# Optimization experiments

Hardware: AMD Instinct MI355X
Metric: run time of the kernel (lower is better)

The kernel has to match this reference:

```python
import jax, jax.numpy as jnp
import numpy as np

DICT = 32768
TOP_K = 128
LN_EPS = 1e-5


def setup_inputs() -> dict:
    key = jax.random.key(0)
    k_x, k_we, k_be, k_wd, k_bd = jax.random.split(key, 5)
    B, S, D = 4, 2048, 768
    x = jax.random.normal(k_x, (B, S, D), dtype=jnp.float32)
    # nn.Linear stores weight as [out, in]; init scaled roughly like orthogonal gains
    W_enc = jax.random.normal(k_we, (DICT, D), dtype=jnp.float32) / np.sqrt(D)
    b_enc = jax.random.normal(k_be, (DICT,), dtype=jnp.float32) * 0.01
    W_dec = jax.random.normal(k_wd, (D, DICT), dtype=jnp.float32) * (0.1 / np.sqrt(DICT))
    b_dec = jax.random.normal(k_bd, (D,), dtype=jnp.float32) * 0.01
    ln_gamma = jnp.ones((DICT,), dtype=jnp.float32)
    ln_beta = jnp.zeros((DICT,), dtype=jnp.float32)
    return {"x": x, "W_enc": W_enc, "b_enc": b_enc, "ln_gamma": ln_gamma,
            "ln_beta": ln_beta, "W_dec": W_dec, "b_dec": b_dec}


def _layernorm(z, gamma, beta):
    mu = jnp.mean(z, axis=-1, keepdims=True)
    var = jnp.mean(jnp.square(z - mu), axis=-1, keepdims=True)
    return (z - mu) * jax.lax.rsqrt(var + LN_EPS) * gamma + beta


def _top_k_activation(z, k):
    # keep top-k values per row, zero elsewhere (scatter, like torch.scatter_)
    vals, idx = jax.lax.top_k(z, k)            # [B,S,k]
    out = jnp.zeros_like(z)
    return jnp.put_along_axis(out, idx, vals, axis=-1, inplace=False)


def reference(x, W_enc, b_enc, ln_gamma, ln_beta, W_dec, b_dec):
    # encoder: [B,S,D] @ [D,DICT] -> [B,S,DICT]
    z = jnp.einsum("bsd,fd->bsf", x, W_enc) + b_enc
    z = _layernorm(z, ln_gamma, ln_beta)
    z = jax.nn.relu(z)
    features = _top_k_activation(z, TOP_K)      # [B,S,DICT], mostly zero
    output = jnp.einsum("bsf,df->bsd", features, W_dec) + b_dec  # [B,S,D]
    return (output, features)
```

## Files before the change

kernel.cpp:

```cpp
#include <hip/hip_runtime.h>
#include <hip/hip_bf16.h>

#define R_TOT  8192
#define DIM    768
#define FDICT  32768
#define TOPK   128
#define LN_EPS 1e-5f
#define BAND_M 0.12f
#define BAND_CAP 192

using f32x4  = __attribute__((ext_vector_type(4))) float;
using short8 = __attribute__((ext_vector_type(8))) short;

__device__ inline short f2bf(float f) {
    __hip_bfloat16 h = __float2bfloat16(f);
    return *reinterpret_cast<short*>(&h);
}
__device__ inline float bf2f(short s) {
    return __uint_as_float(((unsigned)(unsigned short)s) << 16);
}
__device__ inline void load_lds16(const void* g, void* l) {
    __builtin_amdgcn_global_load_lds(
        (const __attribute__((address_space(1))) unsigned int*)g,
        (__attribute__((address_space(3))) unsigned int*)l, 16, 0, 0);
}

__global__ __launch_bounds__(256) void prep_fused(
    const float* __restrict__ x, const float* __restrict__ Wenc,
    const float* __restrict__ Wdec, const float* __restrict__ gamma,
    const float* __restrict__ beta, unsigned short* __restrict__ Xb,
    unsigned short* __restrict__ Wb, unsigned short* __restrict__ WdTb,
    float* __restrict__ gbinfo)
{
    __shared__ float tile[32][33];
    const int b = blockIdx.x;
    const int t = threadIdx.x;

    if (b < 1536) {
        const int n8 = R_TOT * DIM / 8;
        for (int g = b * 256 + t; g < n8; g += 1536 * 256) {
            const float4 a = ((const float4*)x)[g * 2];
            const float4 c = ((const float4*)x)[g * 2 + 1];
            short8 v;
            v[0] = f2bf(a.x); v[1] = f2bf(a.y); v[2] = f2bf(a.z); v[3] = f2bf(a.w);
            v[4] = f2bf(c.x); v[5] = f2bf(c.y); v[6] = f2bf(c.z); v[7] = f2bf(c.w);
            ((short8*)Xb)[g] = v;
        }
    } else if (b < 3584) {
        const int n8 = FDICT * DIM / 8;
        for (int g = (b - 1536) * 256 + t; g < n8; g += 2048 * 256) {
            const float4 a = ((const float4*)Wenc)[g * 2];
            const float4 c = ((const float4*)Wenc)[g * 2 + 1];
            short8 v;
            v[0] = f2bf(a.x); v[1] = f2bf(a.y); v[2] = f2bf(a.z); v[3] = f2bf(a.w);
            v[4] = f2bf(c.x); v[5] = f2bf(c.y); v[6] = f2bf(c.z); v[7] = f2bf(c.w);
            ((short8*)Wb)[g] = v;
        }
    } else if (b < 3584 + 24576) {
        const int b2 = b - 3584;
        const int fx = (b2 & 1023) * 32;
        const int dy = (b2 >> 10) * 32;
        const int tx = t & 31;
        const int ty = t >> 5;
        for (int i = ty; i < 32; i += 8)
            tile[i][tx] = Wdec[(size_t)(dy + i) * FDICT + fx + tx];
        __syncthreads();
        for (int i = ty; i < 32; i += 8)
            WdTb[(size_t)(fx + i) * DIM + dy + tx] = (unsigned short)f2bf(tile[tx][i]);
    } else {
        float* rr = &tile[0][0];
        const int w = t >> 6;
        float gmn = 1e30f, gmx = -1e30f, bmn = 1e30f, bmx = -1e30f;
        for (int i = t; i < FDICT / 4; i += 256) {
            const float4 g4 = ((const float4*)gamma)[i];
            const float4 b4 = ((const float4*)beta)[i];
            gmn = fminf(gmn, fminf(fminf(g4.x, g4.y), fminf(g4.z, g4.w)));
            gmx = fmaxf(gmx, fmaxf(fmaxf(g4.x, g4.y), fmaxf(g4.z, g4.w)));
            bmn = fminf(bmn, fminf(fminf(b4.x, b4.y), fminf(b4.z, b4.w)));
            bmx = fmaxf(bmx, fmaxf(fmaxf(b4.x, b4.y), fmaxf(b4.z, b4.w)));
        }
#pragma unroll
        for (int o = 32; o > 0; o >>= 1) {
            gmn = fminf(gmn, __shfl_down(gmn, o, 64));
            gmx = fmaxf(gmx, __shfl_down(gmx, o, 64));
            bmn = fminf(bmn, __shfl_down(bmn, o, 64));
            bmx = fmaxf(bmx, __shfl_down(bmx, o, 64));
        }
        if ((t & 63) == 0) {
            rr[w * 4 + 0] = gmn; rr[w * 4 + 1] = gmx;
            rr[w * 4 + 2] = bmn; rr[w * 4 + 3] = bmx;
        }
        __syncthreads();
        if (t == 0) {
            float a = rr[0], b_ = rr[1], c = rr[2], d = rr[3];
            for (int i = 1; i < 4; ++i) {
                a = fminf(a, rr[i * 4 + 0]); b_ = fmaxf(b_, rr[i * 4 + 1]);
                c = fminf(c, rr[i * 4 + 2]); d = fmaxf(d, rr[i * 4 + 3]);
            }
            gbinfo[0] = fmaxf(fabsf(a), fabsf(b_));
            gbinfo[1] = fmaxf(fabsf(c), fabsf(d));
            gbinfo[2] = (a == b_ && c == d) ? 1.f : 0.f;
            gbinfo[3] = b_;
            gbinfo[4] = d;
        }
    }
}

#define READ_A(P)                                                              \
    af00 = *(const short8*)&Sb[abase + (2*(P))*1024 + sw0];                    \
    af01 = *(const short8*)&Sb[abase + (2*(P))*1024 + sw1];                    \
    af10 = *(const short8*)&Sb[abase + (2*(P)+1)*1024 + sw0];                  \
    af11 = *(const short8*)&Sb[abase + (2*(P)+1)*1024 + sw1];

#define DO_MFMA(P)                                                             \
    __builtin_amdgcn_s_setprio(1);                                             \
    _Pragma("unroll")                                                          \
    for (int n = 0; n < 4; ++n) {                                              \
        acc[2*(P)][n]   = __builtin_amdgcn_mfma_f32_16x16x32_bf16(af00, bf0[n], acc[2*(P)][n],   0,0,0); \
        acc[2*(P)][n]   = __builtin_amdgcn_mfma_f32_16x16x32_bf16(af01, bf1[n], acc[2*(P)][n],   0,0,0); \
        acc[2*(P)+1][n] = __builtin_amdgcn_mfma_f32_16x16x32_bf16(af10, bf0[n], acc[2*(P)+1][n], 0,0,0); \
        acc[2*(P)+1][n] = __builtin_amdgcn_mfma_f32_16x16x32_bf16(af11, bf1[n], acc[2*(P)+1][n], 0,0,0); \
    }                                                                          \
    __builtin_amdgcn_s_setprio(0);

__global__ __launch_bounds__(512, 2) void enc_gemm(
    const unsigned short* __restrict__ Xb, const unsigned short* __restrict__ Wb,
    const float* __restrict__ benc, unsigned short* __restrict__ Zb,
    float* __restrict__ featZero)
{
    __shared__ __align__(16) unsigned short S[65536];

    const int t = threadIdx.x;
    const int w = t >> 6, l = t & 63;

    const int cpx = (int)gridDim.x >> 3;
    const int swz = ((int)blockIdx.x & 7) * cpx + ((int)blockIdx.x >> 3);
    const long bm = (long)(swz >> 7) * 256;
    const long bn = (long)(swz & 127) * 256;

    const int wm = w >> 2, wn = w & 3;
    const int lrow = l & 15, l4 = l >> 4;

    const int sw0 = ((l4     ) ^ (lrow & 7)) * 8;
    const int sw1 = ((4 + l4 ) ^ (lrow & 7)) * 8;
    const int abase = wm * 8192 + lrow * 64;
    const int bbase = 16384 + wn * 4096 + lrow * 64;

    const int rh0 = w * 16 + (l >> 3);
    const int rh1 = rh0 + 8;
    const int gsl = ((l & 7) ^ (l >> 3)) * 8;
    const unsigned short* pA00 = Xb + (bm +       rh0) * DIM + gsl;
    const unsigned short* pA01 = Xb + (bm +       rh1) * DIM + gsl;
    const unsigned short* pA10 = Xb + (bm + 128 + rh0) * DIM + gsl;
    const unsigned short* pA11 = Xb + (bm + 128 + rh1) * DIM + gsl;
    const unsigned short* pB00 = Wb + (bn +       rh0) * DIM + gsl;
    const unsigned short* pB01 = Wb + (bn +       rh1) * DIM + gsl;
    const unsigned short* pB10 = Wb + (bn + 128 + rh0) * DIM + gsl;
    const unsigned short* pB11 = Wb + (bn + 128 + rh1) * DIM + gsl;
    const int d00 = w * 1024;
    const int d01 = w * 1024 + 512;

    f32x4* zp = featZero ? ((f32x4*)featZero + (size_t)blockIdx.x * 16384) : nullptr;
    const f32x4 z4 = (f32x4){0.f, 0.f, 0.f, 0.f};

    f32x4 acc[8][4];
#pragma unroll
    for (int m = 0; m < 8; ++m)
#pragma unroll
        for (int n = 0; n < 4; ++n) acc[m][n] = (f32x4){0.f, 0.f, 0.f, 0.f};

    load_lds16(pA00, S + d00);
    load_lds16(pA01, S + d01);
    load_lds16(pA10, S + 8192 + d00);
    load_lds16(pA11, S + 8192 + d01);
    load_lds16(pB00, S + 16384 + d00);
    load_lds16(pB01, S + 16384 + d01);
    load_lds16(pB10, S + 16384 + 8192 + d00);
    load_lds16(pB11, S + 16384 + 8192 + d01);
    pA00 += 64; pA01 += 64; pA10 += 64; pA11 += 64;
    pB00 += 64; pB01 += 64; pB10 += 64; pB11 += 64;

    short8 bf0[4], bf1[4];
    short8 af00, af01, af10, af11;

#pragma unroll 1
    for (int kt = 0; kt < 12; ++kt) {
        const unsigned short* Sb = S + (kt & 1) * 32768;
        unsigned short*       Sn = S + ((kt & 1) ^ 1) * 32768;

        if (kt < 11) {
            load_lds16(pA00, Sn + d00);
            load_lds16(pA01, Sn + d01);
            load_lds16(pA10, Sn + 8192 + d00);
            load_lds16(pA11, Sn + 8192 + d01);
            asm volatile("s_waitcnt vmcnt(4)" ::: "memory");
        } else {
            asm volatile("s_waitcnt vmcnt(0)" ::: "memory");
        }
        __builtin_amdgcn_s_barrier();

        if (zp) {
            const int base = kt * 3;
#pragma unroll
            for (int i = 0; i < 3; ++i) {
                const int s = base + i;
                if (s < 32) __builtin_nontemporal_store(z4, zp + t + s * 512);
            }
        }

#pragma unroll
        for (int n = 0; n < 4; ++n) {
            bf0[n] = *(const short8*)&Sb[bbase + n * 1024 + sw0];
            bf1[n] = *(const short8*)&Sb[bbase + n * 1024 + sw1];
        }
        READ_A(0)
        DO_MFMA(0)
        asm volatile("" ::: "memory");
        __builtin_amdgcn_s_barrier();

        READ_A(1)
        if (kt < 11) {
            load_lds16(pB00, Sn + 16384 + d00);
            load_lds16(pB01, Sn + 16384 + d01);
            load_lds16(pB10, Sn + 16384 + 8192 + d00);
            load_lds16(pB11, Sn + 16384 + 8192 + d01);
        }
        asm volatile("" ::: "memory");
        __builtin_amdgcn_s_barrier();
        DO_MFMA(1)
        asm volatile("" ::: "memory");
        __builtin_amdgcn_s_barrier();

        READ_A(2)
        asm volatile("" ::: "memory");
        __builtin_amdgcn_s_barrier();
        DO_MFMA(2)
        asm volatile("" ::: "memory");
        __builtin_amdgcn_s_barrier();

        READ_A(3)
        asm volatile("" ::: "memory");
        __builtin_amdgcn_s_barrier();
        DO_MFMA(3)
        asm volatile("" ::: "memory");
        __builtin_amdgcn_s_barrier();

        pA00 += 64; pA01 += 64; pA10 += 64; pA11 += 64;
        pB00 += 64; pB01 += 64; pB10 += 64; pB11 += 64;
    }

    __syncthreads();
    float bias[4];
#pragma unroll
    for (int n = 0; n < 4; ++n) bias[n] = benc[bn + wn * 64 + n * 16 + lrow];
    unsigned short* Cs = S;
#pragma unroll
    for (int m = 0; m < 8; ++m)
#pragma unroll
        for (int n = 0; n < 4; ++n)
#pragma unroll
            for (int q = 0; q < 4; ++q)
                Cs[(wm * 128 + m * 16 + l4 * 4 + q) * 256 + wn * 64 + n * 16 + lrow] =
                    (unsigned short)f2bf(acc[m][n][q] + bias[n]);
    __syncthreads();
#pragma unroll
    for (int it = 0; it < 16; ++it) {
        const int g = t + it * 512;
        const int row = g >> 5;
        const int c8 = (g & 31) * 8;
        const short8 v = *(const short8*)&Cs[row * 256 + c8];
        __builtin_nontemporal_store(v, (short8*)&Zb[(bm + row) * FDICT + bn + c8]);
    }
}

__global__ __launch_bounds__(1024) void topk_select(
    const unsigned short* __restrict__ Zb, const float* __restrict__ gamma,
    const float* __restrict__ beta, const float* __restrict__ gbinfo,
    int* __restrict__ sel_idx, float* __restrict__ sel_val,
    int* __restrict__ band_idx, int* __restrict__ cdef, int* __restrict__ nband,
    float* __restrict__ muarr, float* __restrict__ sinvarr)
{
    __shared__ float    redf[32];
    __shared__ unsigned cacc[16];
    __shared__ unsigned scomp[2];

    const int t = threadIdx.x;
    const int w = t >> 6;
    const long r = blockIdx.x;

    if (t < 16) cacc[t] = 0u;
    if (t == 16) { scomp[0] = 0u; scomp[1] = 0u; }

    unsigned u[32];
    float sum = 0.f, sumsq = 0.f;
    const short8* Z8 = (const short8*)(Zb + r * (size_t)FDICT);
#pragma unroll
    for (int q = 0; q < 4; ++q) {
        const short8 v = Z8[q * 1024 + t];
#pragma unroll
        for (int j = 0; j < 8; ++j) {
            const float f = bf2f(v[j]);
            u[q * 8 + j] = __float_as_uint(f);
            sum += f; sumsq += f * f;
        }
    }
#pragma unroll
    for (int o = 32; o > 0; o >>= 1) {
        sum   += __shfl_down(sum, o, 64);
        sumsq += __shfl_down(sumsq, o, 64);
    }
    if ((t & 63) == 0) { redf[w] = sum; redf[16 + w] = sumsq; }
    __syncthreads();
    float s_ = 0.f, sq_ = 0.f;
#pragma unroll
    for (int i = 0; i < 16; ++i) { s_ += redf[i]; sq_ += redf[16 + i]; }
    const float mu = s_ / (float)FDICT;
    float var = sq_ / (float)FDICT - mu * mu;
    if (var < 0.f) var = 0.f;
    const float sinv = 1.f / sqrtf(var + LN_EPS);

    const float g0 = gbinfo[3], b0 = gbinfo[4];
    const bool uniform = (gbinfo[2] != 0.f) && (g0 > 0.f) && (g0 <= 2.f);

    if (uniform) {
        const float gs = sinv * g0;
#pragma unroll
        for (int i = 0; i < 32; ++i)
            u[i] = __float_as_uint(fmaxf(
                fmaf(__uint_as_float(u[i]) - mu, gs, b0), 0.f));
    } else {
#pragma unroll
        for (int q = 0; q < 4; ++q) {
            const size_t base = (size_t)(q * 1024 + t) * 8;
            const float4 g4a = *(const float4*)(gamma + base);
            const float4 g4b = *(const float4*)(gamma + base + 4);
            const float4 b4a = *(const float4*)(beta + base);
            const float4 b4b = *(const float4*)(beta + base + 4);
            const float gs[8] = {g4a.x, g4a.y, g4a.z, g4a.w, g4b.x, g4b.y, g4b.z, g4b.w};
            const float bs[8] = {b4a.x, b4a.y, b4a.z, b4a.w, b4b.x, b4b.y, b4b.z, b4b.w};
#pragma unroll
            for (int j = 0; j < 8; ++j) {
                const int i = q * 8 + j;
                u[i] = __float_as_uint(fmaxf(
                    fmaf((__uint_as_float(u[i]) - mu) * sinv, gs[j], bs[j]), 0.f));
            }
        }
    }

    float Tf = 0.f;
    bool got = false;
    int nextacc = 0;
    if (uniform) {
        const float Vh = fmaf(2.6601f, g0, b0);
        const float h  = 0.25f * g0;
        float lo = Vh - h, hi = Vh + h;
        unsigned pc = 0;
#pragma unroll
        for (int i = 0; i < 32; ++i) {
            const float a = __uint_as_float(u[i]);
            pc += (a > lo) ? 1u : 0u;
            pc += (a > hi) ? 0x10000u : 0u;
        }
#pragma unroll
        for (int o = 32; o > 0; o >>= 1) pc += __shfl_down(pc, o, 64);
        if ((t & 63) == 0) atomicAdd(&cacc[0], pc);
        __syncthreads();
        const unsigned clo = cacc[0] & 0xFFFFu, chi = cacc[0] >> 16;
        if (clo >= TOPK && chi < TOPK) {
#pragma unroll 1
            for (int it = 1; it <= 3; ++it) {
                const float thr = 0.5f * (lo + hi);
                unsigned cnt = 0;
#pragma unroll
                for (int i = 0; i < 32; ++i)
                    cnt += (__uint_as_float(u[i]) > thr) ? 1u : 0u;
#pragma unroll
                for (int o = 32; o > 0; o >>= 1) cnt += __shfl_down(cnt, o, 64);
                if ((t & 63) == 0) atomicAdd(&cacc[it], cnt);
                __syncthreads();
                if (cacc[it] >= TOPK) lo = thr; else hi = thr;
            }
            Tf = 0.5f * (lo + hi);
            got = true;
        }
        nextacc = 4;
    }
    if (!got) {
        __syncthreads();
        float vmax = 0.f;
#pragma unroll
        for (int i = 0; i < 32; ++i) vmax = fmaxf(vmax, __uint_as_float(u[i]));
#pragma unroll
        for (int o = 32; o > 0; o >>= 1) vmax = fmaxf(vmax, __shfl_down(vmax, o, 64));
        if ((t & 63) == 0) redf[w] = vmax;
        __syncthreads();
        float mx = 0.f;
#pragma unroll
        for (int i = 0; i < 16; ++i) mx = fmaxf(mx, redf[i]);
        float lo = 0.f, hi = mx + 1e-6f;
#pragma unroll 1
        for (int it = 0; it < 12; ++it) {
            const float thr = 0.5f * (lo + hi);
            unsigned cnt = 0;
#pragma unroll
            for (int i = 0; i < 32; ++i)
                cnt += (__uint_as_float(u[i]) > thr) ? 1u : 0u;
#pragma unroll
            for (int o = 32; o > 0; o >>= 1) cnt += __shfl_down(cnt, o, 64);
            if ((t & 63) == 0) atomicAdd(&cacc[nextacc + it], cnt);
            __syncthreads();
            if (cacc[nextacc + it] >= TOPK) lo = thr; else hi = thr;
        }
        Tf = 0.5f * (lo + hi);
    }

    const float thi = Tf + BAND_M, tlo = Tf - BAND_M;

#pragma unroll
    for (int i = 0; i < 32; ++i) {
        const float a = __uint_as_float(u[i]);
        const int idx = ((i >> 3) * 1024 + t) * 8 + (i & 7);
        if (a > thi) {
            const unsigned s2 = atomicAdd(&scomp[0], 1u);
            sel_idx[r * TOPK + s2] = idx;
            sel_val[r * TOPK + s2] = a;
        } else if (a >= tlo) {
            const unsigned s2 = atomicAdd(&scomp[1], 1u);
            if (s2 < BAND_CAP) band_idx[r * BAND_CAP + s2] = idx;
        }
    }
    __syncthreads();
    if (t == 0) {
        cdef[r]  = (int)scomp[0];
        int nb = (int)scomp[1]; if (nb > BAND_CAP) nb = BAND_CAP;
        nband[r] = nb;
        muarr[r] = mu; sinvarr[r] = sinv;
    }
}

__global__ __launch_bounds__(256) void refine_select(
    const float* __restrict__ X, const float* __restrict__ Wenc,
    const float* __restrict__ benc, const float* __restrict__ gamma,
    const float* __restrict__ beta, const int* __restrict__ band_idx,
    const int* __restrict__ cdef, const int* __restrict__ nband,
    const float* __restrict__ muarr, const float* __restrict__ sinvarr,
    int* __restrict__ sel_idx, float* __restrict__ sel_val,
    float* __restrict__ feat)
{
    __shared__ float xs[DIM];
    __shared__ float cval[BAND_CAP];
    __shared__ int   cidx[BAND_CAP];
    __shared__ int   scnt;
    const int t = threadIdx.x;
    const long r = blockIdx.x;
    const int w = t >> 6, l = t & 63;

    for (int i = t; i < DIM; i += 256) xs[i] = X[r * DIM + i];
    if (t == 0) scnt = 0;
    const int nb = nband[r];
    const int cd = cdef[r];
    int need = TOPK - cd; if (need > nb) need = nb;
    const double mu = (double)muarr[r], sinv = (double)sinvarr[r];

    if (feat && t < cd)
        feat[r * (size_t)FDICT + sel_idx[r * TOPK + t]] = sel_val[r * TOPK + t];
    __syncthreads();

    for (int c = w; c < nb; c += 4) {
        const int fi = band_idx[r * BAND_CAP + c];
        const float* wr = Wenc + (size_t)fi * DIM;
        double s = 0.0;
        for (int k = l; k < DIM; k += 64) s = fma((double)xs[k], (double)wr[k], s);
#pragma unroll
        for (int o = 32; o > 0; o >>= 1) s += __shfl_down(s, o, 64);
        if (l == 0) {
            const double z = s + (double)benc[fi];
            const double a = (z - mu) * sinv * (double)gamma[fi] + (double)beta[fi];
            cval[c] = fmaxf((float)a, 0.f);
            cidx[c] = fi;
        }
    }
    __syncthreads();
    if (t < nb) {
        const float v = cval[t];
        const int id = cidx[t];
        int rank = 0;
        for (int j = 0; j < nb; ++j) {
            const float vj = cval[j];
            rank += (vj > v) || (vj == v && cidx[j] < id);
        }
        if (rank < need) {
            const int s = atomicAdd(&scnt, 1);
            sel_idx[r * TOPK + cd + s] = id;
            sel_val[r * TOPK + cd + s] = v;
            if (feat) feat[r * (size_t)FDICT + id] = v;
        }
    }
}

__global__ __launch_bounds__(384) void decode(
    const int* __restrict__ sel_idx, const float* __restrict__ sel_val,
    const unsigned short* __restrict__ WdTb, const float* __restrict__ bdec,
    float* __restrict__ out)
{
    __shared__ int   sidx[TOPK];
    __shared__ float sval[TOPK];
    const int t = threadIdx.x;
    const long r = blockIdx.x;
    if (t < TOPK) { sidx[t] = sel_idx[r * TOPK + t]; sval[t] = sel_val[r * TOPK + t]; }
    __syncthreads();
    const float2 b2 = *(const float2*)(bdec + t * 2);
    float a0 = b2.x, a1 = b2.y;
    for (int j = 0; j < TOPK; ++j) {
        const unsigned wp = *(const unsigned*)(WdTb + (size_t)sidx[j] * DIM + t * 2);
        const float v = sval[j];
        a0 = fmaf(v, __uint_as_float((wp & 0xFFFFu) << 16), a0);
        a1 = fmaf(v, __uint_as_float(wp & 0xFFFF0000u), a1);
    }
    float2 o2; o2.x = a0; o2.y = a1;
    *(float2*)(out + r * DIM + t * 2) = o2;
}

__global__ __launch_bounds__(1024) void featfill(
    const int* __restrict__ sel_idx, const float* __restrict__ sel_val,
    float* __restrict__ feat)
{
    const int t = threadIdx.x;
    const long r = blockIdx.x;
    const f32x4 z4 = (f32x4){0.f, 0.f, 0.f, 0.f};
    f32x4* row4 = (f32x4*)(feat + r * FDICT);
    for (int i = t; i < FDICT / 4; i += 1024)
        __builtin_nontemporal_store(z4, &row4[i]);
    __syncthreads();
    if (t < TOPK)
        feat[r * FDICT + sel_idx[r * TOPK + t]] = sel_val[r * TOPK + t];
}

extern "C" void kernel_launch(void* const* d_in, const int* in_sizes, int n_in,
                              void* d_out, int out_size, void* d_ws, size_t ws_size,
                              hipStream_t stream)
{
    const float* x     = (const float*)d_in[0];
    const float* Wenc  = (const float*)d_in[1];
    const float* benc  = (const float*)d_in[2];
    const float* gamma = (const float*)d_in[3];
    const float* beta  = (const float*)d_in[4];
    const float* Wdec  = (const float*)d_in[5];
    const float* bdec  = (const float*)d_in[6];

    float* out  = (float*)d_out;
    float* feat = out + (size_t)R_TOT * DIM;

    unsigned short* Xb = (unsigned short*)out;

    char* ws = (char*)d_ws;
    int*   sidx  = (int*)ws;
    float* sval  = (float*)(ws + (size_t)R_TOT * TOPK * 4);
    int*   bidx  = (int*)(ws + (size_t)R_TOT * TOPK * 8);
    int*   cdef  = (int*)(ws + (size_t)R_TOT * (TOPK * 8 + BAND_CAP * 4));
    int*   nbnd  = cdef + R_TOT;
    float* muarr = (float*)(nbnd + R_TOT);
    float* sinva = muarr + R_TOT;
    float* gbinfo = sinva + R_TOT;

    const size_t WS_NEED = 624ull << 20;
    const bool big = (ws_size >= WS_NEED);

    unsigned short* Zb, *Wb, *WdTb;
    if (big) {
        Zb   = (unsigned short*)(ws + (16ull << 20));
        Wb   = (unsigned short*)(ws + (528ull << 20));
        WdTb = (unsigned short*)(ws + (576ull << 20));
    } else {
        Zb   = (unsigned short*)feat;
        Wb   = (unsigned short*)((char*)feat + 536870912ull);
        WdTb = (unsigned short*)((char*)feat + 587202560ull);
    }
    float* featArg = big ? feat : nullptr;

    prep_fused<<<1536 + 2048 + 24576 + 1, 256, 0, stream>>>(
        x, Wenc, Wdec, gamma, beta, Xb, Wb, WdTb, gbinfo);
    enc_gemm<<<4096, 512, 0, stream>>>(Xb, Wb, benc, Zb, featArg);
    topk_select<<<R_TOT, 1024, 0, stream>>>(Zb, gamma, beta, gbinfo,
                                            sidx, sval, bidx, cdef, nbnd,
                                            muarr, sinva);
    refine_select<<<R_TOT, 256, 0, stream>>>(x, Wenc, benc, gamma, beta,
                                             bidx, cdef, nbnd, muarr, sinva,
                                             sidx, sval, featArg);
    decode<<<R_TOT, 384, 0, stream>>>(sidx, sval, WdTb, bdec, out);
    if (!big)
        featfill<<<R_TOT, 1024, 0, stream>>>(sidx, sval, feat);
}
```

Measured before the change: 1.794 ms.

## Process four rows per top-k block with LDS prefetch of next row

The top-k select kernel now handles four consecutive rows per 1024-thread block. Each row is staged into a 64 KB LDS buffer with direct global-to-LDS loads. The next row's load is issued as soon as the current row has been copied into registers, so the HBM read overlaps with the LayerNorm, threshold-search and compaction work. The grid shrinks by four and LDS use per block grows, which lowers the number of resident blocks and trades occupancy-based latency hiding for explicit prefetch.

```diff
diff --git a/kernel.cpp b/kernel.cpp
--- a/kernel.cpp
+++ b/kernel.cpp
@@ -24,6 +24,9 @@
         (const __attribute__((address_space(1))) unsigned int*)g,
         (__attribute__((address_space(3))) unsigned int*)l, 16, 0, 0);
 }
+#define LGKM0() do { asm volatile("s_waitcnt lgkmcnt(0)" ::: "memory"); \
+                     __builtin_amdgcn_sched_barrier(0); } while (0)
+#define BAR()   __builtin_amdgcn_s_barrier()
 
 __global__ __launch_bounds__(256) void prep_fused(
     const float* __restrict__ x, const float* __restrict__ Wenc,
@@ -280,161 +283,191 @@
     int* __restrict__ band_idx, int* __restrict__ cdef, int* __restrict__ nband,
     float* __restrict__ muarr, float* __restrict__ sinvarr)
 {
+    __shared__ __align__(16) unsigned short rowbuf[FDICT];
     __shared__ float    redf[32];
     __shared__ unsigned cacc[16];
     __shared__ unsigned scomp[2];
 
     const int t = threadIdx.x;
     const int w = t >> 6;
-    const long r = blockIdx.x;
-
-    if (t < 16) cacc[t] = 0u;
-    if (t == 16) { scomp[0] = 0u; scomp[1] = 0u; }
-
-    unsigned u[32];
-    float sum = 0.f, sumsq = 0.f;
-    const short8* Z8 = (const short8*)(Zb + r * (size_t)FDICT);
-#pragma unroll
-    for (int q = 0; q < 4; ++q) {
-        const short8 v = Z8[q * 1024 + t];
-#pragma unroll
-        for (int j = 0; j < 8; ++j) {
-            const float f = bf2f(v[j]);
-            u[q * 8 + j] = __float_as_uint(f);
-            sum += f; sumsq += f * f;
-        }
-    }
-#pragma unroll
-    for (int o = 32; o > 0; o >>= 1) {
-        sum   += __shfl_down(sum, o, 64);
-        sumsq += __shfl_down(sumsq, o, 64);
-    }
-    if ((t & 63) == 0) { redf[w] = sum; redf[16 + w] = sumsq; }
-    __syncthreads();
-    float s_ = 0.f, sq_ = 0.f;
-#pragma unroll
-    for (int i = 0; i < 16; ++i) { s_ += redf[i]; sq_ += redf[16 + i]; }
-    const float mu = s_ / (float)FDICT;
-    float var = sq_ / (float)FDICT - mu * mu;
-    if (var < 0.f) var = 0.f;
-    const float sinv = 1.f / sqrtf(var + LN_EPS);
+    const long r0 = (long)blockIdx.x * 4;
 
     const float g0 = gbinfo[3], b0 = gbinfo[4];
     const bool uniform = (gbinfo[2] != 0.f) && (g0 > 0.f) && (g0 <= 2.f);
 
-    if (uniform) {
-        const float gs = sinv * g0;
-#pragma unroll
-        for (int i = 0; i < 32; ++i)
-            u[i] = __float_as_uint(fmaxf(
-                fmaf(__uint_as_float(u[i]) - mu, gs, b0), 0.f));
-    } else {
+    const int lbase = w * 512;
+    const int goff  = w * 512 + (t & 63) * 8;
+
+    {
+        const unsigned short* src = Zb + r0 * FDICT + goff;
+#pragma unroll
+        for (int q = 0; q < 4; ++q)
+            load_lds16(src + q * 8192, rowbuf + lbase + q * 8192);
+    }
+
+#pragma unroll 1
+    for (int i = 0; i < 4; ++i) {
+        const long r = r0 + i;
+        asm volatile("s_waitcnt vmcnt(0)" ::: "memory");
+        BAR();
+
+        unsigned u[32];
+        float sum = 0.f, sumsq = 0.f;
 #pragma unroll
         for (int q = 0; q < 4; ++q) {
-            const size_t base = (size_t)(q * 1024 + t) * 8;
-            const float4 g4a = *(const float4*)(gamma + base);
-            const float4 g4b = *(const float4*)(gamma + base + 4);
-            const float4 b4a = *(const float4*)(beta + base);
-            const float4 b4b = *(const float4*)(beta + base + 4);
-            const float gs[8] = {g4a.x, g4a.y, g4a.z, g4a.w, g4b.x, g4b.y, g4b.z, g4b.w};
-            const float bs[8] = {b4a.x, b4a.y, b4a.z, b4a.w, b4b.x, b4b.y, b4b.z, b4b.w};
+            const short8 v = *(const short8*)&rowbuf[q * 8192 + t * 8];
 #pragma unroll
             for (int j = 0; j < 8; ++j) {
-                const int i = q * 8 + j;
-                u[i] = __float_as_uint(fmaxf(
-                    fmaf((__uint_as_float(u[i]) - mu) * sinv, gs[j], bs[j]), 0.f));
-            }
-        }
-    }
-
-    float Tf = 0.f;
-    bool got = false;
-    int nextacc = 0;
-    if (uniform) {
-        const float Vh = fmaf(2.6601f, g0, b0);
-        const float h  = 0.25f * g0;
-        float lo = Vh - h, hi = Vh + h;
-        unsigned pc = 0;
-#pragma unroll
-        for (int i = 0; i < 32; ++i) {
-            const float a = __uint_as_float(u[i]);
-            pc += (a > lo) ? 1u : 0u;
-            pc += (a > hi) ? 0x10000u : 0u;
-        }
-#pragma unroll
-        for (int o = 32; o > 0; o >>= 1) pc += __shfl_down(pc, o, 64);
-        if ((t & 63) == 0) atomicAdd(&cacc[0], pc);
-        __syncthreads();
-        const unsigned clo = cacc[0] & 0xFFFFu, chi = cacc[0] >> 16;
-        if (clo >= TOPK && chi < TOPK) {
+                const float f = bf2f(v[j]);
+                u[q * 8 + j] = __float_as_uint(f);
+                sum += f; sumsq += f * f;
+            }
+        }
+        LGKM0();
+        BAR();
+        if (t < 16) cacc[t] = 0u;
+        if (t == 16) { scomp[0] = 0u; scomp[1] = 0u; }
+        if (i < 3) {
+            const unsigned short* src = Zb + (r + 1) * FDICT + goff;
+#pragma unroll
+            for (int q = 0; q < 4; ++q)
+                load_lds16(src + q * 8192, rowbuf + lbase + q * 8192);
+        }
+
+#pragma unroll
+        for (int o = 32; o > 0; o >>= 1) {
+            sum   += __shfl_down(sum, o, 64);
+            sumsq += __shfl_down(sumsq, o, 64);
+        }
+        if ((t & 63) == 0) { redf[w] = sum; redf[16 + w] = sumsq; }
+        LGKM0();
+        BAR();
+        float s_ = 0.f, sq_ = 0.f;
+#pragma unroll
+        for (int k = 0; k < 16; ++k) { s_ += redf[k]; sq_ += redf[16 + k]; }
+        const float mu = s_ / (float)FDICT;
+        float var = sq_ / (float)FDICT - mu * mu;
+        if (var < 0.f) var = 0.f;
+        const float sinv = 1.f / sqrtf(var + LN_EPS);
+
+        if (uniform) {
+            const float gs = sinv * g0;
+#pragma unroll
+            for (int k = 0; k < 32; ++k)
+                u[k] = __float_as_uint(fmaxf(
+                    fmaf(__uint_as_float(u[k]) - mu, gs, b0), 0.f));
+        } else {
+#pragma unroll
+            for (int q = 0; q < 4; ++q) {
+                const size_t base = (size_t)(q * 1024 + t) * 8;
+                const float4 g4a = *(const float4*)(gamma + base);
+                const float4 g4b = *(const float4*)(gamma + base + 4);
+                const float4 b4a = *(const float4*)(beta + base);
+                const float4 b4b = *(const float4*)(beta + base + 4);
+                const float gs[8] = {g4a.x, g4a.y, g4a.z, g4a.w, g4b.x, g4b.y, g4b.z, g4b.w};
+                const float bs[8] = {b4a.x, b4a.y, b4a.z, b4a.w, b4b.x, b4b.y, b4b.z, b4b.w};
+#pragma unroll
+                for (int j = 0; j < 8; ++j) {
+                    const int k = q * 8 + j;
+                    u[k] = __float_as_uint(fmaxf(
+                        fmaf((__uint_as_float(u[k]) - mu) * sinv, gs[j], bs[j]), 0.f));
+                }
+            }
+        }
+
+        float Tf = 0.f;
+        bool got = false;
+        int nextacc = 0;
+        if (uniform) {
+            const float Vh = fmaf(2.6601f, g0, b0);
+            const float h  = 0.25f * g0;
+            float lo = Vh - h, hi = Vh + h;
+            unsigned pc = 0;
+#pragma unroll
+            for (int k = 0; k < 32; ++k) {
+                const float a = __uint_as_float(u[k]);
+                pc += (a > lo) ? 1u : 0u;
+                pc += (a > hi) ? 0x10000u : 0u;
+            }
+#pragma unroll
+            for (int o = 32; o > 0; o >>= 1) pc += __shfl_down(pc, o, 64);
+            if ((t & 63) == 0) atomicAdd(&cacc[0], pc);
+            LGKM0();
+            BAR();
+            const unsigned clo = cacc[0] & 0xFFFFu, chi = cacc[0] >> 16;
+            if (clo >= TOPK && chi < TOPK) {
 #pragma unroll 1
-            for (int it = 1; it <= 3; ++it) {
+                for (int it = 1; it <= 3; ++it) {
+                    const float thr = 0.5f * (lo + hi);
+                    unsigned cnt = 0;
+#pragma unroll
+                    for (int k = 0; k < 32; ++k)
+                        cnt += (__uint_as_float(u[k]) > thr) ? 1u : 0u;
+#pragma unroll
+                    for (int o = 32; o > 0; o >>= 1) cnt += __shfl_down(cnt, o, 64);
+                    if ((t & 63) == 0) atomicAdd(&cacc[it], cnt);
+                    LGKM0();
+                    BAR();
+                    if (cacc[it] >= TOPK) lo = thr; else hi = thr;
+                }
+                Tf = 0.5f * (lo + hi);
+                got = true;
+            }
+            nextacc = 4;
+        }
+        if (!got) {
+            float vmax = 0.f;
+#pragma unroll
+            for (int k = 0; k < 32; ++k) vmax = fmaxf(vmax, __uint_as_float(u[k]));
+#pragma unroll
+            for (int o = 32; o > 0; o >>= 1) vmax = fmaxf(vmax, __shfl_down(vmax, o, 64));
+            if ((t & 63) == 0) redf[w] = vmax;
+            LGKM0();
+            BAR();
+            float mx = 0.f;
+#pragma unroll
+            for (int k = 0; k < 16; ++k) mx = fmaxf(mx, redf[k]);
+            float lo = 0.f, hi = mx + 1e-6f;
+#pragma unroll 1
+            for (int it = 0; it < 12; ++it) {
                 const float thr = 0.5f * (lo + hi);
                 unsigned cnt = 0;
 #pragma unroll
-                for (int i = 0; i < 32; ++i)
-                    cnt += (__uint_as_float(u[i]) > thr) ? 1u : 0u;
+                for (int k = 0; k < 32; ++k)
+                    cnt += (__uint_as_float(u[k]) > thr) ? 1u : 0u;
 #pragma unroll
                 for (int o = 32; o > 0; o >>= 1) cnt += __shfl_down(cnt, o, 64);
-                if ((t & 63) == 0) atomicAdd(&cacc[it], cnt);
-                __syncthreads();
-                if (cacc[it] >= TOPK) lo = thr; else hi = thr;
+                if ((t & 63) == 0) atomicAdd(&cacc[nextacc + it], cnt);
+                LGKM0();
+                BAR();
+                if (cacc[nextacc + it] >= TOPK) lo = thr; else hi = thr;
             }
             Tf = 0.5f * (lo + hi);
-            got = true;
-        }
-        nextacc = 4;
-    }
-    if (!got) {
-        __syncthreads();
-        float vmax = 0.f;
-#pragma unroll
-        for (int i = 0; i < 32; ++i) vmax = fmaxf(vmax, __uint_as_float(u[i]));
-#pragma unroll
-        for (int o = 32; o > 0; o >>= 1) vmax = fmaxf(vmax, __shfl_down(vmax, o, 64));
-        if ((t & 63) == 0) redf[w] = vmax;
-        __syncthreads();
-        float mx = 0.f;
-#pragma unroll
-        for (int i = 0; i < 16; ++i) mx = fmaxf(mx, redf[i]);
-        float lo = 0.f, hi = mx + 1e-6f;
-#pragma unroll 1
-        for (int it = 0; it < 12; ++it) {
-            const float thr = 0.5f * (lo + hi);
-            unsigned cnt = 0;
-#pragma unroll
-            for (int i = 0; i < 32; ++i)
-                cnt += (__uint_as_float(u[i]) > thr) ? 1u : 0u;
-#pragma unroll
-            for (int o = 32; o > 0; o >>= 1) cnt += __shfl_down(cnt, o, 64);
-            if ((t & 63) == 0) atomicAdd(&cacc[nextacc + it], cnt);
-            __syncthreads();
-            if (cacc[nextacc + it] >= TOPK) lo = thr; else hi = thr;
-        }
-        Tf = 0.5f * (lo + hi);
-    }
-
-    const float thi = Tf + BAND_M, tlo = Tf - BAND_M;
-
-#pragma unroll
-    for (int i = 0; i < 32; ++i) {
-        const float a = __uint_as_float(u[i]);
-        const int idx = ((i >> 3) * 1024 + t) * 8 + (i & 7);
-        if (a > thi) {
-            const unsigned s2 = atomicAdd(&scomp[0], 1u);
-            sel_idx[r * TOPK + s2] = idx;
-            sel_val[r * TOPK + s2] = a;
-        } else if (a >= tlo) {
-            const unsigned s2 = atomicAdd(&scomp[1], 1u);
-            if (s2 < BAND_CAP) band_idx[r * BAND_CAP + s2] = idx;
-        }
-    }
-    __syncthreads();
-    if (t == 0) {
-        cdef[r]  = (int)scomp[0];
-        int nb = (int)scomp[1]; if (nb > BAND_CAP) nb = BAND_CAP;
-        nband[r] = nb;
-        muarr[r] = mu; sinvarr[r] = sinv;
+        }
+
+        const float thi = Tf + BAND_M, tlo = Tf - BAND_M;
+
+#pragma unroll
+        for (int k = 0; k < 32; ++k) {
+            const float a = __uint_as_float(u[k]);
+            const int idx = ((k >> 3) * 1024 + t) * 8 + (k & 7);
+            if (a > thi) {
+                const unsigned s2 = atomicAdd(&scomp[0], 1u);
+                sel_idx[r * TOPK + s2] = idx;
+                sel_val[r * TOPK + s2] = a;
+            } else if (a >= tlo) {
+                const unsigned s2 = atomicAdd(&scomp[1], 1u);
+                if (s2 < BAND_CAP) band_idx[r * BAND_CAP + s2] = idx;
+            }
+        }
+        LGKM0();
+        BAR();
+        if (t == 0) {
+            cdef[r]  = (int)scomp[0];
+            int nb = (int)scomp[1]; if (nb > BAND_CAP) nb = BAND_CAP;
+            nband[r] = nb;
+            muarr[r] = mu; sinvarr[r] = sinv;
+        }
     }
 }
 
@@ -581,9 +614,9 @@
     prep_fused<<<1536 + 2048 + 24576 + 1, 256, 0, stream>>>(
         x, Wenc, Wdec, gamma, beta, Xb, Wb, WdTb, gbinfo);
     enc_gemm<<<4096, 512, 0, stream>>>(Xb, Wb, benc, Zb, featArg);
-    topk_select<<<R_TOT, 1024, 0, stream>>>(Zb, gamma, beta, gbinfo,
-                                            sidx, sval, bidx, cdef, nbnd,
-                                            muarr, sinva);
+    topk_select<<<R_TOT / 4, 1024, 0, stream>>>(Zb, gamma, beta, gbinfo,
+                                                sidx, sval, bidx, cdef, nbnd,
+                                                muarr, sinva);
     refine_select<<<R_TOT, 256, 0, stream>>>(x, Wenc, benc, gamma, beta,
                                              bidx, cdef, nbnd, muarr, sinva,
                                              sidx, sval, featArg);
```

Measured after the change: 1.793 ms. About the same (-0.1%).
